# Kernel tuning notes

Measured on AMD Instinct MI355X. Metric: run time of the kernel, lower is better.

The kernel has to match this reference:

```python
import jax, jax.numpy as jnp
import numpy as np

N_NODES = 50000


def gat_layer(x, src, dst, W, att_s, att_d, b, concat):
    # PyG GATConv (eval mode): h = x W reshaped to [N, H, C]
    H, C = att_s.shape
    h = (x @ W).reshape(-1, H, C)                      # [N, H, C]
    a_s = (h * att_s).sum(-1)                          # [N, H]
    a_d = (h * att_d).sum(-1)                          # [N, H]
    e = jax.nn.leaky_relu(a_s[src] + a_d[dst], 0.2)    # [E, H]
    # scatter-softmax over destination nodes
    m = jax.ops.segment_max(e, dst, num_segments=N_NODES)
    alpha = jnp.exp(e - m[dst])
    denom = jax.ops.segment_sum(alpha, dst, num_segments=N_NODES)
    alpha = alpha / denom[dst]                         # [E, H]
    msg = h[src] * alpha[:, :, None]                   # [E, H, C]
    out = jax.ops.segment_sum(msg, dst, num_segments=N_NODES)  # [N, H, C]
    out = out.reshape(N_NODES, H * C) if concat else out.mean(axis=1)
    return out + b


def setup_inputs() -> dict:
    key = jax.random.key(0)
    ks = jax.random.split(key, 16)
    F_IN, HID, HEADS, NCLS, E = 512, 64, 4, 40, 800000
    x = jax.random.normal(ks[0], (N_NODES, F_IN), dtype=jnp.float32)
    edge_index = jax.random.randint(ks[1], (2, E), 0, N_NODES, dtype=jnp.int32)

    def glorot(k, shape):
        fan = shape[0]
        return jax.random.normal(k, shape, dtype=jnp.float32) / np.sqrt(fan)

    d1 = HID * HEADS  # 256
    return {
        "x": x,
        "edge_index": edge_index,
        "W1": glorot(ks[2], (F_IN, d1)),
        "as1": glorot(ks[3], (HEADS, HID)),
        "ad1": glorot(ks[4], (HEADS, HID)),
        "b1": jnp.zeros((d1,), jnp.float32),
        "W2": glorot(ks[5], (d1, d1)),
        "as2": glorot(ks[6], (HEADS, HID)),
        "ad2": glorot(ks[7], (HEADS, HID)),
        "b2": jnp.zeros((d1,), jnp.float32),
        "W3": glorot(ks[8], (d1, NCLS)),
        "as3": glorot(ks[9], (1, NCLS)),
        "ad3": glorot(ks[10], (1, NCLS)),
        "b3": jnp.zeros((NCLS,), jnp.float32),
    }


def reference(x, edge_index, W1, as1, ad1, b1, W2, as2, ad2, b2, W3, as3, ad3, b3):
    # add self-loops (PyG GATConv default)
    loops = jnp.arange(N_NODES, dtype=edge_index.dtype)
    src = jnp.concatenate([edge_index[0], loops])
    dst = jnp.concatenate([edge_index[1], loops])
    h = jax.nn.elu(gat_layer(x, src, dst, W1, as1, ad1, b1, True))
    h = jax.nn.elu(gat_layer(h, src, dst, W2, as2, ad2, b2, True))
    out = gat_layer(h, src, dst, W3, as3, ad3, b3, False)
    return out
```

## Files before the change

### kernel.cpp

```cpp
#include <hip/hip_runtime.h>
#include <stdint.h>

#define NN 50000
#define NB 196

typedef unsigned short u16;
typedef _Float16 f16;
typedef __attribute__((ext_vector_type(8))) _Float16 half8;
typedef __attribute__((ext_vector_type(4))) _Float16 half4;
typedef __attribute__((ext_vector_type(4))) float f32x4;


__global__ void count_k(const int* __restrict__ dst, int* __restrict__ cnt, int E){
  int i = blockIdx.x * 256 + threadIdx.x;
  int tot = E + NN;
  if (i >= tot) return;
  int d = (i < E) ? dst[i] : (i - E);
  atomicAdd(&cnt[d], 1);
}

__global__ __launch_bounds__(256) void scan_part_k(const int* __restrict__ cnt,
                                                   int* __restrict__ bsum){
  __shared__ int lds[256];
  int tid = threadIdx.x;
  int idx = blockIdx.x * 256 + tid;
  lds[tid] = (idx < NN) ? cnt[idx] : 0;
  __syncthreads();
#pragma unroll
  for (int off = 128; off >= 1; off >>= 1){
    if (tid < off) lds[tid] += lds[tid + off];
    __syncthreads();
  }
  if (tid == 0) bsum[blockIdx.x] = lds[0];
}

__global__ __launch_bounds__(256) void scan_top_k(const int* __restrict__ bsum,
                                                  int* __restrict__ boff,
                                                  int* __restrict__ row_ptr){
  __shared__ int lds[256];
  int tid = threadIdx.x;
  int v = (tid < NB) ? bsum[tid] : 0;
  lds[tid] = v;
  __syncthreads();
#pragma unroll
  for (int off = 1; off < 256; off <<= 1){
    int t = (tid >= off) ? lds[tid - off] : 0;
    __syncthreads();
    lds[tid] += t;
    __syncthreads();
  }
  if (tid < NB) boff[tid] = lds[tid] - v;
  if (tid == 255) row_ptr[NN] = lds[255];
}

__global__ __launch_bounds__(256) void scan_fin_k(const int* __restrict__ cnt,
                                                  const int* __restrict__ boff,
                                                  int* __restrict__ row_ptr,
                                                  int* __restrict__ cursor){
  __shared__ int lds[256];
  int tid = threadIdx.x;
  int idx = blockIdx.x * 256 + tid;
  int v = (idx < NN) ? cnt[idx] : 0;
  lds[tid] = v;
  __syncthreads();
#pragma unroll
  for (int off = 1; off < 256; off <<= 1){
    int t = (tid >= off) ? lds[tid - off] : 0;
    __syncthreads();
    lds[tid] += t;
    __syncthreads();
  }
  if (idx < NN){
    int r = boff[blockIdx.x] + lds[tid] - v;
    row_ptr[idx] = r;
    cursor[idx]  = r;
  }
}

__global__ void scatter_k(const int* __restrict__ src, const int* __restrict__ dst,
                          int* __restrict__ cursor, int* __restrict__ csr, int E){
  int i = blockIdx.x * 256 + threadIdx.x;
  int tot = E + NN;
  if (i >= tot) return;
  int s, d;
  if (i < E){ s = src[i]; d = dst[i]; } else { s = i - E; d = i - E; }
  int pos = atomicAdd(&cursor[d], 1);
  csr[pos] = s;
}


__global__ void transpose_k(const float* __restrict__ W, f16* __restrict__ Wt, int K, int N){
  int i = blockIdx.x * 256 + threadIdx.x;
  if (i >= K * N) return;
  int n = i / K, k = i - n * K;
  Wt[i] = (f16)W[k * N + n];
}


template<bool A_FP32>
__global__ __launch_bounds__(256) void gemm_tile_k(const void* __restrict__ Aptr,
                                                   const f16* __restrict__ Bt,
                                                   f16* __restrict__ C,
                                                   int M, int N, int K){
  __shared__ f16 As[128 * 32];
  __shared__ f16 Bs[128 * 32];
  const int tid  = threadIdx.x;
  const int wave = tid >> 6, lane = tid & 63;
  const int quad = lane >> 4, l16 = lane & 15;
  const int wm = wave >> 1, wn = wave & 1;
  const int m0 = blockIdx.x * 128, n0 = blockIdx.y * 128;
  const int srow = tid >> 2;
  const int sc   = tid & 3;

  f32x4 acc[4][4] = {};

  for (int k0 = 0; k0 < K; k0 += 32){
#pragma unroll
    for (int rep = 0; rep < 2; rep++){
      int row = rep * 64 + srow;
      int gm = m0 + row;
      half8 va = {0,0,0,0,0,0,0,0};
      if (gm < M){
        if (A_FP32){
          const float* A = (const float*)Aptr + (size_t)gm * K + k0 + sc * 8;
          const f32x4 f0 = *(const f32x4*)(A);
          const f32x4 f1 = *(const f32x4*)(A + 4);
          va[0] = (f16)f0.x; va[1] = (f16)f0.y; va[2] = (f16)f0.z; va[3] = (f16)f0.w;
          va[4] = (f16)f1.x; va[5] = (f16)f1.y; va[6] = (f16)f1.z; va[7] = (f16)f1.w;
        } else {
          va = *(const half8*)((const f16*)Aptr + (size_t)gm * K + k0 + sc * 8);
        }
      }
      *(half8*)(&As[(((row >> 4) * 64) + sc * 16 + (row & 15)) * 8]) = va;
    }
#pragma unroll
    for (int rep = 0; rep < 2; rep++){
      int row = rep * 64 + srow;
      half8 vb = *(const half8*)(Bt + (size_t)(n0 + row) * K + k0 + sc * 8);
      *(half8*)(&Bs[(((row >> 4) * 64) + sc * 16 + (row & 15)) * 8]) = vb;
    }

    __syncthreads();
    half8 af[4], bf[4];
#pragma unroll
    for (int i = 0; i < 4; i++)
      af[i] = *(const half8*)(&As[((wm * 4 + i) * 64 + lane) * 8]);
#pragma unroll
    for (int j = 0; j < 4; j++)
      bf[j] = *(const half8*)(&Bs[((wn * 4 + j) * 64 + lane) * 8]);
#pragma unroll
    for (int i = 0; i < 4; i++)
#pragma unroll
      for (int j = 0; j < 4; j++)
        acc[i][j] = __builtin_amdgcn_mfma_f32_16x16x32_f16(af[i], bf[j], acc[i][j], 0, 0, 0);
    __syncthreads();
  }

#pragma unroll
  for (int i = 0; i < 4; i++){
#pragma unroll
    for (int j = 0; j < 4; j++){
      int n = n0 + (wn * 4 + j) * 16 + l16;
#pragma unroll
      for (int r = 0; r < 4; r++){
        int mm = m0 + (wm * 4 + i) * 16 + quad * 4 + r;
        if (mm < M) C[(size_t)mm * N + n] = (f16)acc[i][j][r];
      }
    }
  }
}


__global__ __launch_bounds__(256) void gemm_k(const f16* __restrict__ A,
                                              const f16* __restrict__ Bt,
                                              f16* __restrict__ C,
                                              int M, int N, int K){
  __shared__ f16 As[64 * 40];
  __shared__ f16 Bs[64 * 40];
  const int tid  = threadIdx.x;
  const int wave = tid >> 6, lane = tid & 63;
  const int quad = lane >> 4, l16 = lane & 15;
  const int m0 = blockIdx.x * 64, n0 = blockIdx.y * 64;
  const int srow = tid >> 2;
  const int scol = (tid & 3) * 8;

  f32x4 acc[4] = {};

  for (int k0 = 0; k0 < K; k0 += 32){
    half8 va = {0,0,0,0,0,0,0,0};
    int gm = m0 + srow;
    if (gm < M) va = *(const half8*)(A + (size_t)gm * K + k0 + scol);
    *(half8*)(&As[srow * 40 + scol]) = va;

    half8 vb = {0,0,0,0,0,0,0,0};
    int gn = n0 + srow;
    if (gn < N) vb = *(const half8*)(Bt + (size_t)gn * K + k0 + scol);
    *(half8*)(&Bs[srow * 40 + scol]) = vb;

    __syncthreads();
    half8 af = *(const half8*)(&As[(wave * 16 + l16) * 40 + quad * 8]);
#pragma unroll
    for (int i = 0; i < 4; i++){
      half8 bf = *(const half8*)(&Bs[(i * 16 + l16) * 40 + quad * 8]);
      acc[i] = __builtin_amdgcn_mfma_f32_16x16x32_f16(af, bf, acc[i], 0, 0, 0);
    }
    __syncthreads();
  }

#pragma unroll
  for (int i = 0; i < 4; i++){
    int n = n0 + i * 16 + l16;
#pragma unroll
    for (int r = 0; r < 4; r++){
      int m = m0 + wave * 16 + quad * 4 + r;
      if (m < M && n < N) C[(size_t)m * N + n] = (f16)acc[i][r];
    }
  }
}


__global__ __launch_bounds__(256) void attn4_k(const f16* __restrict__ h,
                                               const float* __restrict__ atts,
                                               const float* __restrict__ attd,
                                               float* __restrict__ a_s,
                                               float* __restrict__ a_d){
  int w = blockIdx.x * 4 + (threadIdx.x >> 6);
  if (w >= NN) return;
  int lane = threadIdx.x & 63;
  const half4 hv = *(const half4*)(h + (size_t)w * 256 + lane * 4);
  const f32x4 sv = *(const f32x4*)(atts + lane * 4);
  const f32x4 dv = *(const f32x4*)(attd + lane * 4);
  float h0 = (float)hv.x, h1 = (float)hv.y, h2 = (float)hv.z, h3 = (float)hv.w;
  float ps = h0 * sv.x + h1 * sv.y + h2 * sv.z + h3 * sv.w;
  float pd = h0 * dv.x + h1 * dv.y + h2 * dv.z + h3 * dv.w;
#pragma unroll
  for (int off = 8; off >= 1; off >>= 1){
    ps += __shfl_xor(ps, off);
    pd += __shfl_xor(pd, off);
  }
  if ((lane & 15) == 0){
    a_s[w * 4 + (lane >> 4)] = ps;
    a_d[w * 4 + (lane >> 4)] = pd;
  }
}

__global__ __launch_bounds__(256) void attn1_k(const f16* __restrict__ h,
                                               const float* __restrict__ atts,
                                               const float* __restrict__ attd,
                                               float* __restrict__ a_s,
                                               float* __restrict__ a_d){
  int w = blockIdx.x * 4 + (threadIdx.x >> 6);
  if (w >= NN) return;
  int lane = threadIdx.x & 63;
  float ps = 0.f, pd = 0.f;
  if (lane < 40){
    float hv = (float)h[(size_t)w * 40 + lane];
    ps = hv * atts[lane];
    pd = hv * attd[lane];
  }
#pragma unroll
  for (int off = 32; off >= 1; off >>= 1){
    ps += __shfl_xor(ps, off);
    pd += __shfl_xor(pd, off);
  }
  if (lane == 0){ a_s[w] = ps; a_d[w] = pd; }
}


__device__ __forceinline__ float lrelu(float e){ return e > 0.f ? e : 0.2f * e; }

__global__ __launch_bounds__(256) void agg4_k(const f16* __restrict__ h,
                                              const float* __restrict__ a_s,
                                              const float* __restrict__ a_d,
                                              const int* __restrict__ row_ptr,
                                              const int* __restrict__ csr,
                                              const float* __restrict__ bias,
                                              f16* __restrict__ out){
  int w = blockIdx.x * 4 + (threadIdx.x >> 6);
  if (w >= NN) return;
  int lane = threadIdx.x & 63;
  int head = lane >> 4;
  float ad = a_d[w * 4 + head];
  int beg = row_ptr[w], end = row_ptr[w + 1];

  float m = -1e30f, denom = 0.f;
  float acc0 = 0.f, acc1 = 0.f, acc2 = 0.f, acc3 = 0.f;

  int s0 = csr[beg];
  int s1 = csr[(beg + 1 < end) ? beg + 1 : beg];
  float e0 = a_s[s0 * 4 + head];
  float e1 = a_s[s1 * 4 + head];
  half4 h0 = *(const half4*)(h + (size_t)s0 * 256 + lane * 4);
  half4 h1 = *(const half4*)(h + (size_t)s1 * 256 + lane * 4);

  for (int j = beg; j < end; j += 2){
    int t0 = (j + 2 < end) ? j + 2 : j;
    int t1 = (j + 3 < end) ? j + 3 : j;
    int sp0 = csr[t0], sp1 = csr[t1];
    float ep0 = a_s[sp0 * 4 + head];
    float ep1 = a_s[sp1 * 4 + head];
    half4 hp0 = *(const half4*)(h + (size_t)sp0 * 256 + lane * 4);
    half4 hp1 = *(const half4*)(h + (size_t)sp1 * 256 + lane * 4);

    float ee0 = lrelu(e0 + ad);
    float ee1 = (j + 1 < end) ? lrelu(e1 + ad) : -1e30f;
    float mn = fmaxf(m, fmaxf(ee0, ee1));
    float cold = __expf(m - mn);
    float al0 = __expf(ee0 - mn);
    float al1 = __expf(ee1 - mn);
    denom = denom * cold + al0 + al1;
    acc0 = acc0 * cold + al0 * (float)h0.x + al1 * (float)h1.x;
    acc1 = acc1 * cold + al0 * (float)h0.y + al1 * (float)h1.y;
    acc2 = acc2 * cold + al0 * (float)h0.z + al1 * (float)h1.z;
    acc3 = acc3 * cold + al0 * (float)h0.w + al1 * (float)h1.w;
    m = mn;
    e0 = ep0; e1 = ep1; h0 = hp0; h1 = hp1;
  }

  float inv = 1.f / fmaxf(denom, 1e-30f);
  float o0 = acc0 * inv + bias[lane * 4 + 0];
  float o1 = acc1 * inv + bias[lane * 4 + 1];
  float o2 = acc2 * inv + bias[lane * 4 + 2];
  float o3 = acc3 * inv + bias[lane * 4 + 3];
  o0 = o0 > 0.f ? o0 : __expf(o0) - 1.f;
  o1 = o1 > 0.f ? o1 : __expf(o1) - 1.f;
  o2 = o2 > 0.f ? o2 : __expf(o2) - 1.f;
  o3 = o3 > 0.f ? o3 : __expf(o3) - 1.f;
  half4 r; r.x = (f16)o0; r.y = (f16)o1; r.z = (f16)o2; r.w = (f16)o3;
  *(half4*)(out + (size_t)w * 256 + lane * 4) = r;
}

__global__ __launch_bounds__(256) void agg1_k(const f16* __restrict__ h,
                                              const float* __restrict__ a_s,
                                              const float* __restrict__ a_d,
                                              const int* __restrict__ row_ptr,
                                              const int* __restrict__ csr,
                                              const float* __restrict__ bias,
                                              float* __restrict__ out){
  int w = blockIdx.x * 4 + (threadIdx.x >> 6);
  if (w >= NN) return;
  int lane = threadIdx.x & 63;
  int cl = (lane < 40) ? lane : 0;
  float ad = a_d[w];
  int beg = row_ptr[w], end = row_ptr[w + 1];

  float m = -1e30f, denom = 0.f, acc = 0.f;

  int s0 = csr[beg];
  int s1 = csr[(beg + 1 < end) ? beg + 1 : beg];
  float e0 = a_s[s0];
  float e1 = a_s[s1];
  float h0 = (float)h[(size_t)s0 * 40 + cl];
  float h1 = (float)h[(size_t)s1 * 40 + cl];

  for (int j = beg; j < end; j += 2){
    int t0 = (j + 2 < end) ? j + 2 : j;
    int t1 = (j + 3 < end) ? j + 3 : j;
    int sp0 = csr[t0], sp1 = csr[t1];
    float ep0 = a_s[sp0];
    float ep1 = a_s[sp1];
    float hp0 = (float)h[(size_t)sp0 * 40 + cl];
    float hp1 = (float)h[(size_t)sp1 * 40 + cl];

    float ee0 = lrelu(e0 + ad);
    float ee1 = (j + 1 < end) ? lrelu(e1 + ad) : -1e30f;
    float mn = fmaxf(m, fmaxf(ee0, ee1));
    float cold = __expf(m - mn);
    float al0 = __expf(ee0 - mn);
    float al1 = __expf(ee1 - mn);
    denom = denom * cold + al0 + al1;
    acc = acc * cold + al0 * h0 + al1 * h1;
    m = mn;
    e0 = ep0; e1 = ep1; h0 = hp0; h1 = hp1;
  }

  if (lane < 40){
    float o = acc / fmaxf(denom, 1e-30f) + bias[lane];
    out[(size_t)w * 40 + lane] = o;
  }
}


extern "C" void kernel_launch(void* const* d_in, const int* in_sizes, int n_in,
                              void* d_out, int out_size, void* d_ws, size_t ws_size,
                              hipStream_t stream){
  const float* x   = (const float*)d_in[0];
  const int*   ei  = (const int*)d_in[1];
  const float* W1  = (const float*)d_in[2];
  const float* as1 = (const float*)d_in[3];
  const float* ad1 = (const float*)d_in[4];
  const float* b1  = (const float*)d_in[5];
  const float* W2  = (const float*)d_in[6];
  const float* as2 = (const float*)d_in[7];
  const float* ad2 = (const float*)d_in[8];
  const float* b2  = (const float*)d_in[9];
  const float* W3  = (const float*)d_in[10];
  const float* as3 = (const float*)d_in[11];
  const float* ad3 = (const float*)d_in[12];
  const float* b3  = (const float*)d_in[13];

  const int E = in_sizes[1] / 2;
  const int ETOT = E + NN;
  const int* src_arr = ei;
  const int* dst_arr = ei + E;

  char* ws = (char*)d_ws;
  size_t off = 0;
  auto alloc = [&](size_t bytes) -> void* {
    void* p = ws + off; off += (bytes + 255) & ~(size_t)255; return p;
  };
  int*   cnt     = (int*)  alloc((size_t)NN * 4);
  int*   row_ptr = (int*)  alloc((size_t)(NN + 1) * 4);
  int*   cursor  = (int*)  alloc((size_t)NN * 4);
  int*   csr     = (int*)  alloc((size_t)ETOT * 4);
  int*   bsum    = (int*)  alloc((size_t)256 * 4);
  int*   boff    = (int*)  alloc((size_t)256 * 4);
  f16*   W1t     = (f16*)  alloc((size_t)512 * 256 * 2);
  f16*   W2t     = (f16*)  alloc((size_t)256 * 256 * 2);
  f16*   W3t     = (f16*)  alloc((size_t)256 * 40 * 2);
  float* a_s     = (float*)alloc((size_t)NN * 4 * 4);
  float* a_d     = (float*)alloc((size_t)NN * 4 * 4);
  f16*   hbuf    = (f16*)  alloc((size_t)NN * 256 * 2);
  f16*   xbuf    = (f16*)  alloc((size_t)NN * 256 * 2);
  (void)ws_size; (void)n_in; (void)out_size;

  hipMemsetAsync(cnt, 0, (size_t)NN * 4, stream);
  int egrid = (ETOT + 255) / 256;
  count_k    <<<egrid, 256, 0, stream>>>(dst_arr, cnt, E);
  scan_part_k<<<NB, 256, 0, stream>>>(cnt, bsum);
  scan_top_k <<<1, 256, 0, stream>>>(bsum, boff, row_ptr);
  scan_fin_k <<<NB, 256, 0, stream>>>(cnt, boff, row_ptr, cursor);
  scatter_k  <<<egrid, 256, 0, stream>>>(src_arr, dst_arr, cursor, csr, E);

  transpose_k<<<(512 * 256 + 255) / 256, 256, 0, stream>>>(W1, W1t, 512, 256);
  transpose_k<<<(256 * 256 + 255) / 256, 256, 0, stream>>>(W2, W2t, 256, 256);
  transpose_k<<<(256 * 40  + 255) / 256, 256, 0, stream>>>(W3, W3t, 256, 40);

  dim3 blk(256);
  dim3 gT((NN + 127) / 128, 2);
  dim3 gC((NN + 63) / 64, 1);
  int nodeblocks = (NN + 3) / 4;

  gemm_tile_k<true> <<<gT, blk, 0, stream>>>(x, W1t, hbuf, NN, 256, 512);
  attn4_k<<<nodeblocks, blk, 0, stream>>>(hbuf, as1, ad1, a_s, a_d);
  agg4_k <<<nodeblocks, blk, 0, stream>>>(hbuf, a_s, a_d, row_ptr, csr, b1, xbuf);

  gemm_tile_k<false><<<gT, blk, 0, stream>>>(xbuf, W2t, hbuf, NN, 256, 256);
  attn4_k<<<nodeblocks, blk, 0, stream>>>(hbuf, as2, ad2, a_s, a_d);
  agg4_k <<<nodeblocks, blk, 0, stream>>>(hbuf, a_s, a_d, row_ptr, csr, b2, xbuf);

  gemm_k<<<gC, blk, 0, stream>>>(xbuf, W3t, hbuf, NN, 40, 256);
  attn1_k<<<nodeblocks, blk, 0, stream>>>(hbuf, as3, ad3, a_s, a_d);
  agg1_k <<<nodeblocks, blk, 0, stream>>>(hbuf, a_s, a_d, row_ptr, csr, b3, (float*)d_out);
}
```

Before: 562.6 us.

## Precompute normalized attention weights per edge before aggregation

Splits the fused online-softmax aggregation into two stages. A new kernel computes the per-destination max and denominator with 16 lanes per node and writes normalized alpha per edge. The aggregation kernels then only do a weighted sum with 4-way unrolled independent gathers, with no exp or rescaling in the loop. This removes the serial exp and rescale dependency chain from the bandwidth-bound gather loop, at the cost of an extra launch and writing and reading an E×4 float alpha buffer per layer.

```diff
diff --git a/kernel.cpp b/kernel.cpp
--- a/kernel.cpp
+++ b/kernel.cpp
@@ -9,6 +9,8 @@
 typedef __attribute__((ext_vector_type(8))) _Float16 half8;
 typedef __attribute__((ext_vector_type(4))) _Float16 half4;
 typedef __attribute__((ext_vector_type(4))) float f32x4;
+
+__device__ __forceinline__ float lrelu(float e){ return e > 0.f ? e : 0.2f * e; }
 
 
 __global__ void count_k(const int* __restrict__ dst, int* __restrict__ cnt, int E){
@@ -267,11 +269,82 @@
 }
 
 
-__device__ __forceinline__ float lrelu(float e){ return e > 0.f ? e : 0.2f * e; }
+__global__ __launch_bounds__(256) void maxden4_k(const float* __restrict__ a_s,
+                                                 const float* __restrict__ a_d,
+                                                 const int* __restrict__ row_ptr,
+                                                 const int* __restrict__ csr,
+                                                 float* __restrict__ alpha){
+  int w = blockIdx.x * 16 + (threadIdx.x >> 4);
+  if (w >= NN) return;
+  int gl = threadIdx.x & 15;
+  int beg = row_ptr[w], end = row_ptr[w + 1];
+  const f32x4 ad = *(const f32x4*)(a_d + (size_t)w * 4);
+
+  float m0=-1e30f,m1=-1e30f,m2=-1e30f,m3=-1e30f;
+  float s0=0.f,s1=0.f,s2=0.f,s3=0.f;
+  for (int j = beg + gl; j < end; j += 16){
+    int s = csr[j];
+    const f32x4 as = *(const f32x4*)(a_s + (size_t)s * 4);
+    float e, mn;
+    e = lrelu(as.x + ad.x); mn = fmaxf(m0, e); s0 = s0*__expf(m0-mn) + __expf(e-mn); m0 = mn;
+    e = lrelu(as.y + ad.y); mn = fmaxf(m1, e); s1 = s1*__expf(m1-mn) + __expf(e-mn); m1 = mn;
+    e = lrelu(as.z + ad.z); mn = fmaxf(m2, e); s2 = s2*__expf(m2-mn) + __expf(e-mn); m2 = mn;
+    e = lrelu(as.w + ad.w); mn = fmaxf(m3, e); s3 = s3*__expf(m3-mn) + __expf(e-mn); m3 = mn;
+  }
+#pragma unroll
+  for (int k = 1; k < 16; k <<= 1){
+    float mo, so, mn;
+    mo=__shfl_xor(m0,k); so=__shfl_xor(s0,k); mn=fmaxf(m0,mo); s0=s0*__expf(m0-mn)+so*__expf(mo-mn); m0=mn;
+    mo=__shfl_xor(m1,k); so=__shfl_xor(s1,k); mn=fmaxf(m1,mo); s1=s1*__expf(m1-mn)+so*__expf(mo-mn); m1=mn;
+    mo=__shfl_xor(m2,k); so=__shfl_xor(s2,k); mn=fmaxf(m2,mo); s2=s2*__expf(m2-mn)+so*__expf(mo-mn); m2=mn;
+    mo=__shfl_xor(m3,k); so=__shfl_xor(s3,k); mn=fmaxf(m3,mo); s3=s3*__expf(m3-mn)+so*__expf(mo-mn); m3=mn;
+  }
+  float i0 = 1.f/fmaxf(s0,1e-30f), i1 = 1.f/fmaxf(s1,1e-30f);
+  float i2 = 1.f/fmaxf(s2,1e-30f), i3 = 1.f/fmaxf(s3,1e-30f);
+
+  for (int j = beg + gl; j < end; j += 16){
+    int s = csr[j];
+    const f32x4 as = *(const f32x4*)(a_s + (size_t)s * 4);
+    f32x4 al;
+    al.x = __expf(lrelu(as.x + ad.x) - m0) * i0;
+    al.y = __expf(lrelu(as.y + ad.y) - m1) * i1;
+    al.z = __expf(lrelu(as.z + ad.z) - m2) * i2;
+    al.w = __expf(lrelu(as.w + ad.w) - m3) * i3;
+    *(f32x4*)(alpha + (size_t)j * 4) = al;
+  }
+}
+
+__global__ __launch_bounds__(256) void maxden1_k(const float* __restrict__ a_s,
+                                                 const float* __restrict__ a_d,
+                                                 const int* __restrict__ row_ptr,
+                                                 const int* __restrict__ csr,
+                                                 float* __restrict__ alpha){
+  int w = blockIdx.x * 16 + (threadIdx.x >> 4);
+  if (w >= NN) return;
+  int gl = threadIdx.x & 15;
+  int beg = row_ptr[w], end = row_ptr[w + 1];
+  const float ad = a_d[w];
+
+  float m = -1e30f, sum = 0.f;
+  for (int j = beg + gl; j < end; j += 16){
+    float e = lrelu(a_s[csr[j]] + ad);
+    float mn = fmaxf(m, e);
+    sum = sum*__expf(m-mn) + __expf(e-mn); m = mn;
+  }
+#pragma unroll
+  for (int k = 1; k < 16; k <<= 1){
+    float mo=__shfl_xor(m,k), so=__shfl_xor(sum,k);
+    float mn=fmaxf(m,mo);
+    sum = sum*__expf(m-mn) + so*__expf(mo-mn); m = mn;
+  }
+  float inv = 1.f/fmaxf(sum,1e-30f);
+  for (int j = beg + gl; j < end; j += 16)
+    alpha[j] = __expf(lrelu(a_s[csr[j]] + ad) - m) * inv;
+}
+
 
 __global__ __launch_bounds__(256) void agg4_k(const f16* __restrict__ h,
-                                              const float* __restrict__ a_s,
-                                              const float* __restrict__ a_d,
+                                              const float* __restrict__ alpha,
                                               const int* __restrict__ row_ptr,
                                               const int* __restrict__ csr,
                                               const float* __restrict__ bias,
@@ -280,48 +353,37 @@
   if (w >= NN) return;
   int lane = threadIdx.x & 63;
   int head = lane >> 4;
-  float ad = a_d[w * 4 + head];
   int beg = row_ptr[w], end = row_ptr[w + 1];
 
-  float m = -1e30f, denom = 0.f;
   float acc0 = 0.f, acc1 = 0.f, acc2 = 0.f, acc3 = 0.f;
-
-  int s0 = csr[beg];
-  int s1 = csr[(beg + 1 < end) ? beg + 1 : beg];
-  float e0 = a_s[s0 * 4 + head];
-  float e1 = a_s[s1 * 4 + head];
-  half4 h0 = *(const half4*)(h + (size_t)s0 * 256 + lane * 4);
-  half4 h1 = *(const half4*)(h + (size_t)s1 * 256 + lane * 4);
-
-  for (int j = beg; j < end; j += 2){
-    int t0 = (j + 2 < end) ? j + 2 : j;
-    int t1 = (j + 3 < end) ? j + 3 : j;
-    int sp0 = csr[t0], sp1 = csr[t1];
-    float ep0 = a_s[sp0 * 4 + head];
-    float ep1 = a_s[sp1 * 4 + head];
-    half4 hp0 = *(const half4*)(h + (size_t)sp0 * 256 + lane * 4);
-    half4 hp1 = *(const half4*)(h + (size_t)sp1 * 256 + lane * 4);
-
-    float ee0 = lrelu(e0 + ad);
-    float ee1 = (j + 1 < end) ? lrelu(e1 + ad) : -1e30f;
-    float mn = fmaxf(m, fmaxf(ee0, ee1));
-    float cold = __expf(m - mn);
-    float al0 = __expf(ee0 - mn);
-    float al1 = __expf(ee1 - mn);
-    denom = denom * cold + al0 + al1;
-    acc0 = acc0 * cold + al0 * (float)h0.x + al1 * (float)h1.x;
-    acc1 = acc1 * cold + al0 * (float)h0.y + al1 * (float)h1.y;
-    acc2 = acc2 * cold + al0 * (float)h0.z + al1 * (float)h1.z;
-    acc3 = acc3 * cold + al0 * (float)h0.w + al1 * (float)h1.w;
-    m = mn;
-    e0 = ep0; e1 = ep1; h0 = hp0; h1 = hp1;
-  }
-
-  float inv = 1.f / fmaxf(denom, 1e-30f);
-  float o0 = acc0 * inv + bias[lane * 4 + 0];
-  float o1 = acc1 * inv + bias[lane * 4 + 1];
-  float o2 = acc2 * inv + bias[lane * 4 + 2];
-  float o3 = acc3 * inv + bias[lane * 4 + 3];
+  int j = beg;
+  for (; j + 4 <= end; j += 4){
+    int s0 = csr[j], s1 = csr[j+1], s2 = csr[j+2], s3 = csr[j+3];
+    float a0 = alpha[(size_t)j*4 + head];
+    float a1 = alpha[(size_t)(j+1)*4 + head];
+    float a2 = alpha[(size_t)(j+2)*4 + head];
+    float a3 = alpha[(size_t)(j+3)*4 + head];
+    half4 v0 = *(const half4*)(h + (size_t)s0*256 + lane*4);
+    half4 v1 = *(const half4*)(h + (size_t)s1*256 + lane*4);
+    half4 v2 = *(const half4*)(h + (size_t)s2*256 + lane*4);
+    half4 v3 = *(const half4*)(h + (size_t)s3*256 + lane*4);
+    acc0 += a0*(float)v0.x + a1*(float)v1.x + a2*(float)v2.x + a3*(float)v3.x;
+    acc1 += a0*(float)v0.y + a1*(float)v1.y + a2*(float)v2.y + a3*(float)v3.y;
+    acc2 += a0*(float)v0.z + a1*(float)v1.z + a2*(float)v2.z + a3*(float)v3.z;
+    acc3 += a0*(float)v0.w + a1*(float)v1.w + a2*(float)v2.w + a3*(float)v3.w;
+  }
+  for (; j < end; j++){
+    int s = csr[j];
+    float a = alpha[(size_t)j*4 + head];
+    half4 v = *(const half4*)(h + (size_t)s*256 + lane*4);
+    acc0 += a*(float)v.x; acc1 += a*(float)v.y;
+    acc2 += a*(float)v.z; acc3 += a*(float)v.w;
+  }
+
+  float o0 = acc0 + bias[lane*4+0];
+  float o1 = acc1 + bias[lane*4+1];
+  float o2 = acc2 + bias[lane*4+2];
+  float o3 = acc3 + bias[lane*4+3];
   o0 = o0 > 0.f ? o0 : __expf(o0) - 1.f;
   o1 = o1 > 0.f ? o1 : __expf(o1) - 1.f;
   o2 = o2 > 0.f ? o2 : __expf(o2) - 1.f;
@@ -331,8 +393,7 @@
 }
 
 __global__ __launch_bounds__(256) void agg1_k(const f16* __restrict__ h,
-                                              const float* __restrict__ a_s,
-                                              const float* __restrict__ a_d,
+                                              const float* __restrict__ alpha,
                                               const int* __restrict__ row_ptr,
                                               const int* __restrict__ csr,
                                               const float* __restrict__ bias,
@@ -341,42 +402,25 @@
   if (w >= NN) return;
   int lane = threadIdx.x & 63;
   int cl = (lane < 40) ? lane : 0;
-  float ad = a_d[w];
   int beg = row_ptr[w], end = row_ptr[w + 1];
 
-  float m = -1e30f, denom = 0.f, acc = 0.f;
-
-  int s0 = csr[beg];
-  int s1 = csr[(beg + 1 < end) ? beg + 1 : beg];
-  float e0 = a_s[s0];
-  float e1 = a_s[s1];
-  float h0 = (float)h[(size_t)s0 * 40 + cl];
-  float h1 = (float)h[(size_t)s1 * 40 + cl];
-
-  for (int j = beg; j < end; j += 2){
-    int t0 = (j + 2 < end) ? j + 2 : j;
-    int t1 = (j + 3 < end) ? j + 3 : j;
-    int sp0 = csr[t0], sp1 = csr[t1];
-    float ep0 = a_s[sp0];
-    float ep1 = a_s[sp1];
-    float hp0 = (float)h[(size_t)sp0 * 40 + cl];
-    float hp1 = (float)h[(size_t)sp1 * 40 + cl];
-
-    float ee0 = lrelu(e0 + ad);
-    float ee1 = (j + 1 < end) ? lrelu(e1 + ad) : -1e30f;
-    float mn = fmaxf(m, fmaxf(ee0, ee1));
-    float cold = __expf(m - mn);
-    float al0 = __expf(ee0 - mn);
-    float al1 = __expf(ee1 - mn);
-    denom = denom * cold + al0 + al1;
-    acc = acc * cold + al0 * h0 + al1 * h1;
-    m = mn;
-    e0 = ep0; e1 = ep1; h0 = hp0; h1 = hp1;
+  float acc = 0.f;
+  int j = beg;
+  for (; j + 4 <= end; j += 4){
+    int s0 = csr[j], s1 = csr[j+1], s2 = csr[j+2], s3 = csr[j+3];
+    float a0 = alpha[j], a1 = alpha[j+1], a2 = alpha[j+2], a3 = alpha[j+3];
+    float v0 = (float)h[(size_t)s0*40 + cl];
+    float v1 = (float)h[(size_t)s1*40 + cl];
+    float v2 = (float)h[(size_t)s2*40 + cl];
+    float v3 = (float)h[(size_t)s3*40 + cl];
+    acc += a0*v0 + a1*v1 + a2*v2 + a3*v3;
+  }
+  for (; j < end; j++){
+    acc += alpha[j] * (float)h[(size_t)csr[j]*40 + cl];
   }
 
   if (lane < 40){
-    float o = acc / fmaxf(denom, 1e-30f) + bias[lane];
-    out[(size_t)w * 40 + lane] = o;
+    out[(size_t)w * 40 + lane] = acc + bias[lane];
   }
 }
 
@@ -420,6 +464,7 @@
   f16*   W3t     = (f16*)  alloc((size_t)256 * 40 * 2);
   float* a_s     = (float*)alloc((size_t)NN * 4 * 4);
   float* a_d     = (float*)alloc((size_t)NN * 4 * 4);
+  float* alpha   = (float*)alloc((size_t)ETOT * 4 * 4);
   f16*   hbuf    = (f16*)  alloc((size_t)NN * 256 * 2);
   f16*   xbuf    = (f16*)  alloc((size_t)NN * 256 * 2);
   (void)ws_size; (void)n_in; (void)out_size;
@@ -440,16 +485,20 @@
   dim3 gT((NN + 127) / 128, 2);
   dim3 gC((NN + 63) / 64, 1);
   int nodeblocks = (NN + 3) / 4;
+  int grpblocks  = (NN + 15) / 16;
 
   gemm_tile_k<true> <<<gT, blk, 0, stream>>>(x, W1t, hbuf, NN, 256, 512);
-  attn4_k<<<nodeblocks, blk, 0, stream>>>(hbuf, as1, ad1, a_s, a_d);
-  agg4_k <<<nodeblocks, blk, 0, stream>>>(hbuf, a_s, a_d, row_ptr, csr, b1, xbuf);
+  attn4_k  <<<nodeblocks, blk, 0, stream>>>(hbuf, as1, ad1, a_s, a_d);
+  maxden4_k<<<grpblocks, blk, 0, stream>>>(a_s, a_d, row_ptr, csr, alpha);
+  agg4_k   <<<nodeblocks, blk, 0, stream>>>(hbuf, alpha, row_ptr, csr, b1, xbuf);
 
   gemm_tile_k<false><<<gT, blk, 0, stream>>>(xbuf, W2t, hbuf, NN, 256, 256);
-  attn4_k<<<nodeblocks, blk, 0, stream>>>(hbuf, as2, ad2, a_s, a_d);
-  agg4_k <<<nodeblocks, blk, 0, stream>>>(hbuf, a_s, a_d, row_ptr, csr, b2, xbuf);
+  attn4_k  <<<nodeblocks, blk, 0, stream>>>(hbuf, as2, ad2, a_s, a_d);
+  maxden4_k<<<grpblocks, blk, 0, stream>>>(a_s, a_d, row_ptr, csr, alpha);
+  agg4_k   <<<nodeblocks, blk, 0, stream>>>(hbuf, alpha, row_ptr, csr, b2, xbuf);
 
   gemm_k<<<gC, blk, 0, stream>>>(xbuf, W3t, hbuf, NN, 40, 256);
-  attn1_k<<<nodeblocks, blk, 0, stream>>>(hbuf, as3, ad3, a_s, a_d);
-  agg1_k <<<nodeblocks, blk, 0, stream>>>(hbuf, a_s, a_d, row_ptr, csr, b3, (float*)d_out);
-}
+  attn1_k  <<<nodeblocks, blk, 0, stream>>>(hbuf, as3, ad3, a_s, a_d);
+  maxden1_k<<<grpblocks, blk, 0, stream>>>(a_s, a_d, row_ptr, csr, alpha);
+  agg1_k   <<<nodeblocks, blk, 0, stream>>>(hbuf, alpha, row_ptr, csr, b3, (float*)d_out);
+}
```

Result: no change. 573.8 us (+2.0%).
